# Optimization experiments

Measured on AMD Instinct MI355X. Metric: run time of the kernel, lower is better.

Reference implementation:

```python
import jax, jax.numpy as jnp
import numpy as np

N, E, G = 50000, 800000, 100
H, C = 4, 64


def _gatv2(x, src, dst, ea, Wl, bl, Wr, br, We, att, bias):
    # PyG GATv2Conv: x_l = lin_l(x) (source side), x_r = lin_r(x) (target side)
    xl = (x @ Wl + bl).reshape(-1, H, C)
    xr = (x @ Wr + br).reshape(-1, H, C)
    e = (ea @ We).reshape(-1, H, C)               # [E,H,C]
    m = jax.nn.leaky_relu(xl[src] + xr[dst] + e, negative_slope=0.2)
    alpha = jnp.einsum('ehc,hc->eh', m, att)      # [E,H]
    amax = jax.ops.segment_max(alpha, dst, num_segments=N)
    amax = jnp.where(jnp.isfinite(amax), amax, jnp.float32(0.0))
    ex = jnp.exp(alpha - amax[dst])
    denom = jax.ops.segment_sum(ex, dst, num_segments=N)
    a = ex / (denom[dst] + jnp.float32(1e-16))    # segment softmax over in-edges
    out = jax.ops.segment_sum(xl[src] * a[..., None], dst, num_segments=N)
    return out.reshape(N, H * C) + bias


def setup_inputs() -> dict:
    key = jax.random.key(0)
    ks = jax.random.split(key, 24)
    lin = lambda k, i, o: (jax.random.normal(k, (i, o), jnp.float32) / np.sqrt(i).astype(np.float32))
    x = jax.random.normal(ks[0], (N, 8), jnp.float32)
    edge_index = jnp.stack([jax.random.randint(ks[1], (E,), 0, N),
                            jax.random.randint(ks[2], (E,), 0, N)])
    edge_attr = jax.random.normal(ks[3], (E, 1), jnp.float32)
    batch = jnp.sort(jax.random.randint(ks[4], (N,), 0, G))
    return dict(
        x=x, edge_index=edge_index, edge_attr=edge_attr, batch=batch,
        enc_W=lin(ks[5], 8, 64), enc_b=jnp.zeros((64,), jnp.float32),
        g1_Wl=lin(ks[6], 64, 256), g1_bl=jnp.zeros((256,), jnp.float32),
        g1_Wr=lin(ks[7], 64, 256), g1_br=jnp.zeros((256,), jnp.float32),
        g1_We=lin(ks[8], 1, 256),
        g1_att=jax.random.normal(ks[9], (H, C), jnp.float32) / np.sqrt(C).astype(np.float32),
        g1_bias=jnp.zeros((256,), jnp.float32),
        g2_Wl=lin(ks[10], 256, 256), g2_bl=jnp.zeros((256,), jnp.float32),
        g2_Wr=lin(ks[11], 256, 256), g2_br=jnp.zeros((256,), jnp.float32),
        g2_We=lin(ks[12], 1, 256),
        g2_att=jax.random.normal(ks[13], (H, C), jnp.float32) / np.sqrt(C).astype(np.float32),
        g2_bias=jnp.zeros((256,), jnp.float32),
        p1_W=lin(ks[14], 256, 128), p1_b=jnp.zeros((128,), jnp.float32),
        ln_g=jnp.ones((128,), jnp.float32), ln_b=jnp.zeros((128,), jnp.float32),
        p2_W=lin(ks[15], 128, 64), p2_b=jnp.zeros((64,), jnp.float32),
    )


def reference(x, edge_index, edge_attr, batch,
              enc_W, enc_b,
              g1_Wl, g1_bl, g1_Wr, g1_br, g1_We, g1_att, g1_bias,
              g2_Wl, g2_bl, g2_Wr, g2_br, g2_We, g2_att, g2_bias,
              p1_W, p1_b, ln_g, ln_b, p2_W, p2_b):
    src, dst = edge_index[0], edge_index[1]
    h = jax.nn.relu(x @ enc_W + enc_b)
    h = jax.nn.relu(_gatv2(h, src, dst, edge_attr, g1_Wl, g1_bl, g1_Wr, g1_br, g1_We, g1_att, g1_bias))
    h = jax.nn.relu(_gatv2(h, src, dst, edge_attr, g2_Wl, g2_bl, g2_Wr, g2_br, g2_We, g2_att, g2_bias))
    # global mean pool over graphs
    sums = jax.ops.segment_sum(h, batch, num_segments=G)
    cnt = jax.ops.segment_sum(jnp.ones((N, 1), h.dtype), batch, num_segments=G)
    p = sums / jnp.maximum(cnt, jnp.float32(1.0))
    # post MLP (dropout is identity in eval)
    z = p @ p1_W + p1_b
    mu = jnp.mean(z, axis=-1, keepdims=True)
    var = jnp.mean(jnp.square(z - mu), axis=-1, keepdims=True)
    z = (z - mu) * jax.lax.rsqrt(var + jnp.float32(1e-5)) * ln_g + ln_b
    z = jax.nn.relu(z)
    return jax.nn.relu(z @ p2_W + p2_b)
```

## Files before the change

### kernel.cpp

```cpp
#include <hip/hip_runtime.h>

#define NH 4
#define CH 64

__device__ __forceinline__ unsigned short f2bf(float f) {
  unsigned b = __float_as_uint(f);
  return (unsigned short)((b + 0x7fffu + ((b >> 16) & 1u)) >> 16);
}
__device__ __forceinline__ float bf2f(unsigned short u) {
  return __uint_as_float(((unsigned)u) << 16);
}

__global__ void encoder_kernel(const float* __restrict__ x, const float* __restrict__ W,
                               const float* __restrict__ b, float* __restrict__ h, int N) {
  int idx = blockIdx.x * blockDim.x + threadIdx.x;
  if (idx >= N * 64) return;
  int n = idx >> 6, j = idx & 63;
  const float* xp = x + n * 8;
  float acc = b[j];
#pragma unroll
  for (int k = 0; k < 8; ++k) acc = fmaf(xp[k], W[k * 64 + j], acc);
  h[idx] = fmaxf(acc, 0.0f);
}

template <int K>
__global__ void lin_lr_kernel(const float* __restrict__ h,
                              const float* __restrict__ Wl, const float* __restrict__ bl,
                              const float* __restrict__ Wr, const float* __restrict__ br,
                              unsigned short* __restrict__ xlb, float* __restrict__ xr, int N) {
  __shared__ float hs[8][K];
  int n0 = blockIdx.x * 8;
  int j = threadIdx.x;
  int nmax = N - n0; if (nmax > 8) nmax = 8;
  for (int idx = j; idx < nmax * K; idx += 256) {
    int m = idx / K, k = idx % K;
    hs[m][k] = h[(size_t)(n0 + m) * K + k];
  }
  __syncthreads();
  float accl[8], accr[8];
  float bjl = bl[j], bjr = br[j];
#pragma unroll
  for (int m = 0; m < 8; ++m) { accl[m] = bjl; accr[m] = bjr; }
  for (int k = 0; k < K; ++k) {
    float wl = Wl[k * 256 + j];
    float wr = Wr[k * 256 + j];
#pragma unroll
    for (int m = 0; m < 8; ++m) {
      accl[m] = fmaf(hs[m][k], wl, accl[m]);
      accr[m] = fmaf(hs[m][k], wr, accr[m]);
    }
  }
  for (int m = 0; m < nmax; ++m) {
    xlb[(size_t)(n0 + m) * 256 + j] = f2bf(accl[m]);
    xr[(size_t)(n0 + m) * 256 + j] = accr[m];
  }
}

__global__ void hist_kernel(const int* __restrict__ dst, int* __restrict__ deg, int E) {
  int e = blockIdx.x * blockDim.x + threadIdx.x;
  if (e < E) atomicAdd(&deg[dst[e]], 1);
}

__global__ void scan_partial_kernel(const int* __restrict__ deg, int* __restrict__ partial, int N) {
  __shared__ int sm[256];
  int t = threadIdx.x;
  int i = blockIdx.x * 256 + t;
  sm[t] = (i < N) ? deg[i] : 0;
  __syncthreads();
#pragma unroll
  for (int s = 128; s > 0; s >>= 1) {
    if (t < s) sm[t] += sm[t + s];
    __syncthreads();
  }
  if (t == 0) partial[blockIdx.x] = sm[0];
}

__global__ void scan_offsets_kernel(int* __restrict__ partial, int nb) {
  __shared__ int sm[256];
  int t = threadIdx.x;
  int v = (t < nb) ? partial[t] : 0;
  sm[t] = v;
  __syncthreads();
#pragma unroll
  for (int off = 1; off < 256; off <<= 1) {
    int a = (t >= off) ? sm[t - off] : 0;
    __syncthreads();
    sm[t] += a;
    __syncthreads();
  }
  if (t < nb) partial[t] = sm[t] - v;
}

__global__ void scan_final_kernel(const int* __restrict__ deg, const int* __restrict__ partial,
                                  int* __restrict__ rowptr, int* __restrict__ cursor, int N, int E) {
  __shared__ int sm[256];
  int t = threadIdx.x;
  int i = blockIdx.x * 256 + t;
  int v = (i < N) ? deg[i] : 0;
  sm[t] = v;
  __syncthreads();
#pragma unroll
  for (int off = 1; off < 256; off <<= 1) {
    int a = (t >= off) ? sm[t - off] : 0;
    __syncthreads();
    sm[t] += a;
    __syncthreads();
  }
  if (i < N) {
    int ex = partial[blockIdx.x] + sm[t] - v;
    rowptr[i] = ex;
    cursor[i] = ex;
  }
  if (i == 0) rowptr[N] = E;
}

__global__ void scatter_build_kernel(const int* __restrict__ src, const int* __restrict__ dst,
                                     const float* __restrict__ ea, int* __restrict__ cursor,
                                     int2* __restrict__ edg, int E) {
  int e = blockIdx.x * blockDim.x + threadIdx.x;
  if (e >= E) return;
  int d = dst[e];
  int pos = atomicAdd(&cursor[d], 1);
  edg[pos] = make_int2(src[e], __float_as_int(ea[e]));
}

__device__ __forceinline__ void edge_accum(const ushort4 xu, const float eav,
                                           const float4 xr4, const float4 We4, const float4 at4,
                                           float4& acc, float& denom) {
  float4 xlv;
  xlv.x = bf2f(xu.x); xlv.y = bf2f(xu.y); xlv.z = bf2f(xu.z); xlv.w = bf2f(xu.w);
  float4 v;
  v.x = fmaf(eav, We4.x, xlv.x + xr4.x);
  v.y = fmaf(eav, We4.y, xlv.y + xr4.y);
  v.z = fmaf(eav, We4.z, xlv.z + xr4.z);
  v.w = fmaf(eav, We4.w, xlv.w + xr4.w);
  v.x = (v.x >= 0.f) ? v.x : 0.2f * v.x;
  v.y = (v.y >= 0.f) ? v.y : 0.2f * v.y;
  v.z = (v.z >= 0.f) ? v.z : 0.2f * v.z;
  v.w = (v.w >= 0.f) ? v.w : 0.2f * v.w;
  float p = v.x * at4.x + v.y * at4.y + v.z * at4.z + v.w * at4.w;
  p += __shfl_xor(p, 1, 64);
  p += __shfl_xor(p, 2, 64);
  p += __shfl_xor(p, 4, 64);
  p += __shfl_xor(p, 8, 64);
  float ex = __expf(p);
  denom += ex;
  acc.x = fmaf(ex, xlv.x, acc.x);
  acc.y = fmaf(ex, xlv.y, acc.y);
  acc.z = fmaf(ex, xlv.z, acc.z);
  acc.w = fmaf(ex, xlv.w, acc.w);
}

template <bool POOL>
__global__ void gat_aggregate_kernel(const int* __restrict__ rowptr,
                                     const int2* __restrict__ edg,
                                     const unsigned short* __restrict__ xlb,
                                     const float* __restrict__ xr,
                                     const float* __restrict__ We,
                                     const float* __restrict__ att,
                                     const float* __restrict__ bias,
                                     float* __restrict__ out,
                                     const int* __restrict__ batch,
                                     float* __restrict__ sums,
                                     float* __restrict__ cnt,
                                     int N) {
  int d = (int)((blockIdx.x * (size_t)blockDim.x + threadIdx.x) >> 6);
  int lane = threadIdx.x & 63;
  if (d >= N) return;
  const ushort4* xlp = (const ushort4*)xlb;
  float4 xr4 = ((const float4*)xr)[(size_t)d * 64 + lane];
  float4 We4 = ((const float4*)We)[lane];
  float4 at4 = ((const float4*)att)[lane];
  int beg = rowptr[d], end = rowptr[d + 1];
  float4 acc = {0.f, 0.f, 0.f, 0.f};
  float denom = 0.f;
  int i = beg;
  for (; i + 1 < end; i += 2) {
    int2 e0 = edg[i], e1 = edg[i + 1];
    ushort4 a0 = xlp[(size_t)e0.x * 64 + lane];
    ushort4 a1 = xlp[(size_t)e1.x * 64 + lane];
    edge_accum(a0, __int_as_float(e0.y), xr4, We4, at4, acc, denom);
    edge_accum(a1, __int_as_float(e1.y), xr4, We4, at4, acc, denom);
  }
  if (i < end) {
    int2 e0 = edg[i];
    ushort4 a0 = xlp[(size_t)e0.x * 64 + lane];
    edge_accum(a0, __int_as_float(e0.y), xr4, We4, at4, acc, denom);
  }
  float inv = 1.f / (denom + 1e-16f);
  float4 b4 = ((const float4*)bias)[lane];
  float4 o;
  o.x = fmaxf(fmaf(acc.x, inv, b4.x), 0.f);
  o.y = fmaxf(fmaf(acc.y, inv, b4.y), 0.f);
  o.z = fmaxf(fmaf(acc.z, inv, b4.z), 0.f);
  o.w = fmaxf(fmaf(acc.w, inv, b4.w), 0.f);
  if (POOL) {
    int g = batch[d];
    float* sg = sums + (size_t)g * 256 + lane * 4;
    atomicAdd(sg + 0, o.x);
    atomicAdd(sg + 1, o.y);
    atomicAdd(sg + 2, o.z);
    atomicAdd(sg + 3, o.w);
    if (lane == 0) atomicAdd(&cnt[g], 1.0f);
  } else {
    ((float4*)out)[(size_t)d * 64 + lane] = o;
  }
}

__global__ void mlp_kernel(const float* __restrict__ sums, const float* __restrict__ cnt,
                           const float* __restrict__ p1W, const float* __restrict__ p1b,
                           const float* __restrict__ lng, const float* __restrict__ lnb,
                           const float* __restrict__ p2W, const float* __restrict__ p2b,
                           float* __restrict__ outp, int G) {
  __shared__ float p[256];
  __shared__ float z[128];
  __shared__ float wsum[2];
  __shared__ float wsum2[2];
  int g = blockIdx.x;
  int t = threadIdx.x;
  float c = fmaxf(cnt[g], 1.0f);
  p[t] = sums[(size_t)g * 256 + t] / c;
  p[t + 128] = sums[(size_t)g * 256 + t + 128] / c;
  __syncthreads();
  float acc = p1b[t];
  for (int k = 0; k < 256; ++k) acc = fmaf(p[k], p1W[k * 128 + t], acc);
  float v = acc;
#pragma unroll
  for (int off = 32; off > 0; off >>= 1) v += __shfl_xor(v, off, 64);
  if ((t & 63) == 0) wsum[t >> 6] = v;
  __syncthreads();
  float mu = (wsum[0] + wsum[1]) * (1.0f / 128.0f);
  float dv = acc - mu;
  float vv = dv * dv;
#pragma unroll
  for (int off = 32; off > 0; off >>= 1) vv += __shfl_xor(vv, off, 64);
  if ((t & 63) == 0) wsum2[t >> 6] = vv;
  __syncthreads();
  float var = (wsum2[0] + wsum2[1]) * (1.0f / 128.0f);
  float zv = dv * rsqrtf(var + 1e-5f) * lng[t] + lnb[t];
  z[t] = fmaxf(zv, 0.0f);
  __syncthreads();
  if (t < 64) {
    float o = p2b[t];
    for (int k = 0; k < 128; ++k) o = fmaf(z[k], p2W[k * 64 + t], o);
    outp[(size_t)g * 64 + t] = fmaxf(o, 0.0f);
  }
}

extern "C" void kernel_launch(void* const* d_in, const int* in_sizes, int n_in,
                              void* d_out, int out_size, void* d_ws, size_t ws_size,
                              hipStream_t stream) {
  const float* x      = (const float*)d_in[0];
  const int*   ei     = (const int*)d_in[1];
  const float* ea     = (const float*)d_in[2];
  const int*   batch  = (const int*)d_in[3];
  const float* enc_W  = (const float*)d_in[4];
  const float* enc_b  = (const float*)d_in[5];
  const float* Wl1    = (const float*)d_in[6];
  const float* bl1    = (const float*)d_in[7];
  const float* Wr1    = (const float*)d_in[8];
  const float* br1    = (const float*)d_in[9];
  const float* We1    = (const float*)d_in[10];
  const float* att1   = (const float*)d_in[11];
  const float* bias1  = (const float*)d_in[12];
  const float* Wl2    = (const float*)d_in[13];
  const float* bl2    = (const float*)d_in[14];
  const float* Wr2    = (const float*)d_in[15];
  const float* br2    = (const float*)d_in[16];
  const float* We2    = (const float*)d_in[17];
  const float* att2   = (const float*)d_in[18];
  const float* bias2  = (const float*)d_in[19];
  const float* p1W    = (const float*)d_in[20];
  const float* p1b    = (const float*)d_in[21];
  const float* lng    = (const float*)d_in[22];
  const float* lnb    = (const float*)d_in[23];
  const float* p2W    = (const float*)d_in[24];
  const float* p2b    = (const float*)d_in[25];
  float* outp = (float*)d_out;

  int N = in_sizes[0] / 8;
  int E = in_sizes[2];
  int G = out_size / 64;
  const int* src = ei;
  const int* dst = ei + E;
  int nb = (N + 255) / 256;

  float* ws      = (float*)d_ws;
  float* h0      = ws;
  float* B1      = h0     + (size_t)N * 64;
  float* B2      = B1     + (size_t)N * 256;
  float* sums    = B2     + (size_t)N * 256;
  float* cnt     = sums   + (size_t)G * 256;
  unsigned short* xlb = (unsigned short*)(cnt + G);
  int2*  edg     = (int2*)(xlb + (size_t)N * 256);
  int*   rowptr  = (int*)(edg + (size_t)E);
  int*   cursor  = rowptr + (size_t)(N + 1);
  int*   partial = cursor + (size_t)N;

  encoder_kernel<<<(N * 64 + 255) / 256, 256, 0, stream>>>(x, enc_W, enc_b, h0, N);

  hipMemsetAsync(cursor, 0, (size_t)N * sizeof(int), stream);
  hist_kernel<<<(E + 255) / 256, 256, 0, stream>>>(dst, cursor, E);
  scan_partial_kernel<<<nb, 256, 0, stream>>>(cursor, partial, N);
  scan_offsets_kernel<<<1, 256, 0, stream>>>(partial, nb);
  scan_final_kernel<<<nb, 256, 0, stream>>>(cursor, partial, rowptr, cursor, N, E);
  scatter_build_kernel<<<(E + 255) / 256, 256, 0, stream>>>(src, dst, ea, cursor, edg, E);

  lin_lr_kernel<64><<<(N + 7) / 8, 256, 0, stream>>>(h0, Wl1, bl1, Wr1, br1, xlb, B1, N);
  gat_aggregate_kernel<false><<<(N + 3) / 4, 256, 0, stream>>>(
      rowptr, edg, xlb, B1, We1, att1, bias1, B2, nullptr, nullptr, nullptr, N);

  lin_lr_kernel<256><<<(N + 7) / 8, 256, 0, stream>>>(B2, Wl2, bl2, Wr2, br2, xlb, B1, N);
  hipMemsetAsync(sums, 0, ((size_t)G * 256 + G) * sizeof(float), stream);
  gat_aggregate_kernel<true><<<(N + 3) / 4, 256, 0, stream>>>(
      rowptr, edg, xlb, B1, We2, att2, bias2, nullptr, batch, sums, cnt, N);

  mlp_kernel<<<G, 128, 0, stream>>>(sums, cnt, p1W, p1b, lng, lnb, p2W, p2b, outp, G);
}
```

Measured before the change: 1.043 ms.

## Pipeline GAT neighbor gathers through LDS with async global_load_lds and fp32 xl

The aggregate kernel now stages each wave's edge metadata into LDS and issues gathers of source-node xl rows through global_load_lds into a 7-slot ring buffer. It uses vmcnt waits so several neighbor loads stay in flight while earlier edges are processed. The bf16 packing of xl is dropped and xl is stored as fp32, which doubles gather traffic per edge but removes the conversions and precision loss. The manual waitcnt-based pipeline is fragile and uses about 32 KB of LDS per block, which may limit occupancy.

```diff
diff --git a/kernel.cpp b/kernel.cpp
--- a/kernel.cpp
+++ b/kernel.cpp
@@ -2,14 +2,6 @@
 
 #define NH 4
 #define CH 64
-
-__device__ __forceinline__ unsigned short f2bf(float f) {
-  unsigned b = __float_as_uint(f);
-  return (unsigned short)((b + 0x7fffu + ((b >> 16) & 1u)) >> 16);
-}
-__device__ __forceinline__ float bf2f(unsigned short u) {
-  return __uint_as_float(((unsigned)u) << 16);
-}
 
 __global__ void encoder_kernel(const float* __restrict__ x, const float* __restrict__ W,
                                const float* __restrict__ b, float* __restrict__ h, int N) {
@@ -27,7 +19,7 @@
 __global__ void lin_lr_kernel(const float* __restrict__ h,
                               const float* __restrict__ Wl, const float* __restrict__ bl,
                               const float* __restrict__ Wr, const float* __restrict__ br,
-                              unsigned short* __restrict__ xlb, float* __restrict__ xr, int N) {
+                              float* __restrict__ xl, float* __restrict__ xr, int N) {
   __shared__ float hs[8][K];
   int n0 = blockIdx.x * 8;
   int j = threadIdx.x;
@@ -51,7 +43,7 @@
     }
   }
   for (int m = 0; m < nmax; ++m) {
-    xlb[(size_t)(n0 + m) * 256 + j] = f2bf(accl[m]);
+    xl[(size_t)(n0 + m) * 256 + j] = accl[m];
     xr[(size_t)(n0 + m) * 256 + j] = accr[m];
   }
 }
@@ -124,11 +116,25 @@
   edg[pos] = make_int2(src[e], __float_as_int(ea[e]));
 }
 
-__device__ __forceinline__ void edge_accum(const ushort4 xu, const float eav,
+typedef const __attribute__((address_space(1))) void* gas_p;
+typedef __attribute__((address_space(3))) void* las_p;
+__device__ __forceinline__ void load_lds16(const void* g, void* l) {
+  __builtin_amdgcn_global_load_lds((gas_p)g, (las_p)l, 16, 0, 0);
+}
+#define WAITVM(v) __builtin_amdgcn_s_waitcnt(0xF70 | (v))
+__device__ __forceinline__ void waitvm_rt(int v) {
+  switch (v) {
+    case 0: WAITVM(0); break;
+    case 1: WAITVM(1); break;
+    case 2: WAITVM(2); break;
+    case 3: WAITVM(3); break;
+    default: WAITVM(4); break;
+  }
+}
+
+__device__ __forceinline__ void edge_accum(const float4 xlv, const float eav,
                                            const float4 xr4, const float4 We4, const float4 at4,
                                            float4& acc, float& denom) {
-  float4 xlv;
-  xlv.x = bf2f(xu.x); xlv.y = bf2f(xu.y); xlv.z = bf2f(xu.z); xlv.w = bf2f(xu.w);
   float4 v;
   v.x = fmaf(eav, We4.x, xlv.x + xr4.x);
   v.y = fmaf(eav, We4.y, xlv.y + xr4.y);
@@ -152,41 +158,69 @@
 }
 
 template <bool POOL>
-__global__ void gat_aggregate_kernel(const int* __restrict__ rowptr,
-                                     const int2* __restrict__ edg,
-                                     const unsigned short* __restrict__ xlb,
-                                     const float* __restrict__ xr,
-                                     const float* __restrict__ We,
-                                     const float* __restrict__ att,
-                                     const float* __restrict__ bias,
-                                     float* __restrict__ out,
-                                     const int* __restrict__ batch,
-                                     float* __restrict__ sums,
-                                     float* __restrict__ cnt,
-                                     int N) {
-  int d = (int)((blockIdx.x * (size_t)blockDim.x + threadIdx.x) >> 6);
+__global__ __launch_bounds__(256) void gat_aggregate_kernel(
+    const int* __restrict__ rowptr, const int2* __restrict__ edg,
+    const float* __restrict__ xl, const float* __restrict__ xr,
+    const float* __restrict__ We, const float* __restrict__ att,
+    const float* __restrict__ bias, float* __restrict__ out,
+    const int* __restrict__ batch, float* __restrict__ sums, float* __restrict__ cnt,
+    int N) {
+  constexpr int P = 7;
+  __shared__ __align__(16) char smem[4 * (1024 + P * 1024)];
+  int wib = threadIdx.x >> 6;
   int lane = threadIdx.x & 63;
+  int d = blockIdx.x * 4 + wib;
   if (d >= N) return;
-  const ushort4* xlp = (const ushort4*)xlb;
+  char* wbase = smem + wib * (1024 + P * 1024);
+  int2* meta = (int2*)wbase;
+  float* slots = (float*)(wbase + 1024);
+
   float4 xr4 = ((const float4*)xr)[(size_t)d * 64 + lane];
   float4 We4 = ((const float4*)We)[lane];
   float4 at4 = ((const float4*)att)[lane];
   int beg = rowptr[d], end = rowptr[d + 1];
   float4 acc = {0.f, 0.f, 0.f, 0.f};
   float denom = 0.f;
-  int i = beg;
-  for (; i + 1 < end; i += 2) {
-    int2 e0 = edg[i], e1 = edg[i + 1];
-    ushort4 a0 = xlp[(size_t)e0.x * 64 + lane];
-    ushort4 a1 = xlp[(size_t)e1.x * 64 + lane];
-    edge_accum(a0, __int_as_float(e0.y), xr4, We4, at4, acc, denom);
-    edge_accum(a1, __int_as_float(e1.y), xr4, We4, at4, acc, denom);
-  }
-  if (i < end) {
-    int2 e0 = edg[i];
-    ushort4 a0 = xlp[(size_t)e0.x * 64 + lane];
-    edge_accum(a0, __int_as_float(e0.y), xr4, We4, at4, acc, denom);
-  }
+
+  for (int cbeg = beg; cbeg < end; cbeg += 128) {
+    int L = end - cbeg; if (L > 128) L = 128;
+    load_lds16((const char*)(edg + cbeg) + lane * 16, meta);
+    WAITVM(0);
+    int F = (L < P - 1) ? L : (P - 1);
+#pragma unroll
+    for (int k = 0; k < P - 1; ++k) {
+      if (k < F) {
+        int s = meta[k].x;
+        load_lds16((const char*)(xl + (size_t)s * 256) + lane * 16, slots + k * 256);
+      }
+    }
+    int j = 0, cs = 0, is_ = F;
+    for (; j <= L - P + 1; ++j) {
+      WAITVM(P - 2);
+      int2 mm = meta[j];
+      float4 a = ((const float4*)(slots + cs * 256))[lane];
+      edge_accum(a, __int_as_float(mm.y), xr4, We4, at4, acc, denom);
+      int nx = j + P - 1;
+      if (nx < L) {
+        int s = meta[nx].x;
+        load_lds16((const char*)(xl + (size_t)s * 256) + lane * 16, slots + is_ * 256);
+        if (++is_ == P) is_ = 0;
+      }
+      if (++cs == P) cs = 0;
+    }
+#pragma unroll
+    for (int k = P - 3; k >= 0; --k) {
+      if (j < L && (L - 1 - j) == k) {
+        waitvm_rt(k);
+        int2 mm = meta[j];
+        float4 a = ((const float4*)(slots + cs * 256))[lane];
+        edge_accum(a, __int_as_float(mm.y), xr4, We4, at4, acc, denom);
+        if (++cs == P) cs = 0;
+        ++j;
+      }
+    }
+  }
+
   float inv = 1.f / (denom + 1e-16f);
   float4 b4 = ((const float4*)bias)[lane];
   float4 o;
@@ -287,12 +321,12 @@
 
   float* ws      = (float*)d_ws;
   float* h0      = ws;
-  float* B1      = h0     + (size_t)N * 64;
+  float* B0      = h0     + (size_t)N * 64;
+  float* B1      = B0     + (size_t)N * 256;
   float* B2      = B1     + (size_t)N * 256;
   float* sums    = B2     + (size_t)N * 256;
   float* cnt     = sums   + (size_t)G * 256;
-  unsigned short* xlb = (unsigned short*)(cnt + G);
-  int2*  edg     = (int2*)(xlb + (size_t)N * 256);
+  int2*  edg     = (int2*)(cnt + G);
   int*   rowptr  = (int*)(edg + (size_t)E);
   int*   cursor  = rowptr + (size_t)(N + 1);
   int*   partial = cursor + (size_t)N;
@@ -306,14 +340,14 @@
   scan_final_kernel<<<nb, 256, 0, stream>>>(cursor, partial, rowptr, cursor, N, E);
   scatter_build_kernel<<<(E + 255) / 256, 256, 0, stream>>>(src, dst, ea, cursor, edg, E);
 
-  lin_lr_kernel<64><<<(N + 7) / 8, 256, 0, stream>>>(h0, Wl1, bl1, Wr1, br1, xlb, B1, N);
+  lin_lr_kernel<64><<<(N + 7) / 8, 256, 0, stream>>>(h0, Wl1, bl1, Wr1, br1, B0, B1, N);
   gat_aggregate_kernel<false><<<(N + 3) / 4, 256, 0, stream>>>(
-      rowptr, edg, xlb, B1, We1, att1, bias1, B2, nullptr, nullptr, nullptr, N);
-
-  lin_lr_kernel<256><<<(N + 7) / 8, 256, 0, stream>>>(B2, Wl2, bl2, Wr2, br2, xlb, B1, N);
+      rowptr, edg, B0, B1, We1, att1, bias1, B2, nullptr, nullptr, nullptr, N);
+
+  lin_lr_kernel<256><<<(N + 7) / 8, 256, 0, stream>>>(B2, Wl2, bl2, Wr2, br2, B0, B1, N);
   hipMemsetAsync(sums, 0, ((size_t)G * 256 + G) * sizeof(float), stream);
   gat_aggregate_kernel<true><<<(N + 3) / 4, 256, 0, stream>>>(
-      rowptr, edg, xlb, B1, We2, att2, bias2, nullptr, batch, sums, cnt, N);
+      rowptr, edg, B0, B1, We2, att2, bias2, nullptr, batch, sums, cnt, N);
 
   mlp_kernel<<<G, 128, 0, stream>>>(sums, cnt, p1W, p1b, lng, lnb, p2W, p2b, outp, G);
 }
```

After: 1.177 ms. +12.9%, slower.
